# Kernel tuning notes

Measured on AMD Instinct MI355X. Metric: run time of the kernel, lower is better.

Reference implementation:

```python
import jax, jax.numpy as jnp
import numpy as np

PI = float(np.pi)


def setup_inputs() -> dict:
    key = jax.random.key(0)
    ks = jax.random.split(key, 10)
    Nt, Nv, Nx, Nx_out, rank = 1024, 128, 512, 2048, 128
    K = 2 * rank + 1  # 257
    x_sample = jnp.linspace(0.0, 10.0 * PI, Nx, dtype=jnp.float32)
    v_sample = jnp.linspace(-8.0, 8.0, Nv, dtype=jnp.float32)
    x_out = jax.random.uniform(ks[0], (Nx_out,), jnp.float32, 0.0, 10.0 * PI)
    f = jax.random.normal(ks[1], (Nt, Nv, Nx), jnp.float32)
    # psi MLP params (Linear stores W as (out,in) in torch; we use (in,out))
    W1 = jax.random.normal(ks[2], (2, 64), jnp.float32) * 0.5
    b1 = jax.random.normal(ks[3], (64,), jnp.float32) * 0.1
    W2 = jax.random.normal(ks[4], (64, 32), jnp.float32) * 0.125
    b2 = jax.random.normal(ks[5], (32,), jnp.float32) * 0.1
    W3 = jax.random.normal(ks[6], (32, K), jnp.float32) * 0.18
    b3 = jax.random.normal(ks[7], (K,), jnp.float32) * 0.1
    return {"x_out": x_out, "f": f, "x_sample": x_sample, "v_sample": v_sample,
            "W1": W1, "b1": b1, "W2": W2, "b2": b2, "W3": W3, "b3": b3}


def _psi_mlp(xv, W1, b1, W2, b2, W3, b3):
    h = jax.nn.relu(xv @ W1 + b1)
    h = jax.nn.relu(h @ W2 + b2)
    return h @ W3 + b3


def reference(x_out, f, x_sample, v_sample, W1, b1, W2, b2, W3, b3):
    Nt, Nv, Nx = f.shape
    K = W3.shape[1]           # 2*rank + 1
    rank = (K - 1) // 2
    w = 2.0 * PI / (x_sample.max() - x_sample.min())
    hx = x_sample[1] - x_sample[0]
    hv = v_sample[1] - v_sample[0]
    # meshgrid indexing='xy': X, V have shape (Nv, Nx)
    X = jnp.broadcast_to(x_sample[None, :], (Nv, Nx))
    V = jnp.broadcast_to(v_sample[:, None], (Nv, Nx))
    xv = jnp.stack([X.reshape(-1), V.reshape(-1)], axis=1)  # (Nv*Nx, 2)
    Psi = _psi_mlp(xv, W1, b1, W2, b2, W3, b3).reshape(Nv, Nx, K)
    # fused contraction replacing broadcast-multiply-reduce: (Nt,Nv,Nx)x(Nv,Nx,K)->(Nt,K)
    weights = jnp.einsum('tvx,vxk->tk', f, Psi) * (hx * hv)
    ks = jnp.arange(1, rank + 1, dtype=x_out.dtype)
    kc = jnp.arange(0, rank + 1, dtype=x_out.dtype)
    phi = jnp.concatenate([jnp.sin(ks[:, None] * w * x_out[None, :]),
                           jnp.cos(kc[:, None] * w * x_out[None, :])], axis=0)  # (K, Nx_out)
    return weights @ phi  # (Nt, Nx_out)
```

## Files before the change

### kernel.cpp

```cpp
#include <hip/hip_runtime.h>
#include <hip/hip_bf16.h>

typedef short v8s __attribute__((ext_vector_type(8)));
typedef float v4f __attribute__((ext_vector_type(4)));

#define NT   1024
#define NVX  65536
#define KTRUE 257
#define KP   272
#define NXO  2048
#define NJ   48
#define NKC  64

static __device__ __forceinline__ unsigned short f2bf(float f) {
  unsigned int u = __float_as_uint(f);
  u += 0x7FFFu + ((u >> 16) & 1u);
  return (unsigned short)(u >> 16);
}

__global__ void k0_prep(const float* __restrict__ W3, const float* __restrict__ b3,
                        float* __restrict__ W3e) {
  int k = threadIdx.x;
  if (k >= KP) return;
  int j = blockIdx.x;
  float val = 0.f;
  if (k < KTRUE) {
    if (j < 32)       val = W3[j*KTRUE + k];
    else if (j == 32) val = b3[k];
  }
  W3e[j*KP + k] = val;
}

__global__ __launch_bounds__(256) void k1_mlp(
    const float* __restrict__ xs, const float* __restrict__ vs,
    const float* __restrict__ W1, const float* __restrict__ b1,
    const float* __restrict__ W2, const float* __restrict__ b2,
    unsigned short* __restrict__ H2T) {
  int vx = blockIdx.x * 256 + threadIdx.x;
  float x = xs[vx & 511];
  float v = vs[vx >> 9];
  float h2[32];
#pragma unroll
  for (int q = 0; q < 8; ++q) {
    float4 t = ((const float4*)b2)[q];
    h2[q*4+0] = t.x; h2[q*4+1] = t.y; h2[q*4+2] = t.z; h2[q*4+3] = t.w;
  }
#pragma unroll 4
  for (int i = 0; i < 64; ++i) {
    float h1 = fmaf(x, W1[i], fmaf(v, W1[64+i], b1[i]));
    h1 = fmaxf(h1, 0.f);
    const float4* w2r = (const float4*)(W2 + i*32);
#pragma unroll
    for (int q = 0; q < 8; ++q) {
      float4 t = w2r[q];
      h2[q*4+0] = fmaf(h1, t.x, h2[q*4+0]);
      h2[q*4+1] = fmaf(h1, t.y, h2[q*4+1]);
      h2[q*4+2] = fmaf(h1, t.z, h2[q*4+2]);
      h2[q*4+3] = fmaf(h1, t.w, h2[q*4+3]);
    }
  }
#pragma unroll
  for (int j = 0; j < 32; ++j)
    H2T[(size_t)j*NVX + vx] = f2bf(fmaxf(h2[j], 0.f));
  H2T[(size_t)32*NVX + vx] = 0x3F80;
}

__global__ __launch_bounds__(256) void k2_gemm(
    const float* __restrict__ f, const unsigned short* __restrict__ H2T,
    float* __restrict__ Gpart) {
  const int tid  = threadIdx.x;
  const int kc   = blockIdx.x >> 4;
  const int mt   = blockIdx.x & 15;
  const int wave = tid >> 6;
  const int lane = tid & 63;
  const int frow = lane & 15;
  const int kg   = (lane >> 4) * 8;
  const int row  = mt*64 + wave*16 + frow;
  const size_t kbase = (size_t)kc * 1024;

  const float* fp = f + (size_t)row * NVX + kbase + kg;
  const unsigned short* bp0 = H2T + (size_t)(frow)      * NVX + kbase + kg;
  const unsigned short* bp1 = H2T + (size_t)(16 + frow) * NVX + kbase + kg;
  const unsigned short* bp2 = H2T + (size_t)(32 + frow) * NVX + kbase + kg;

  v4f acc0 = {0.f,0.f,0.f,0.f}, acc1 = {0.f,0.f,0.f,0.f}, acc2 = {0.f,0.f,0.f,0.f};

#pragma unroll 4
  for (int step = 0; step < 32; ++step) {
    const int o = step * 32;
    float4 fa = *(const float4*)(fp + o);
    float4 fb = *(const float4*)(fp + o + 4);
    union { v8s v; __hip_bfloat162 h[4]; } au;
    au.h[0] = __float22bfloat162_rn(float2{fa.x, fa.y});
    au.h[1] = __float22bfloat162_rn(float2{fa.z, fa.w});
    au.h[2] = __float22bfloat162_rn(float2{fb.x, fb.y});
    au.h[3] = __float22bfloat162_rn(float2{fb.z, fb.w});
    v8s b0 = *(const v8s*)(bp0 + o);
    v8s b1 = *(const v8s*)(bp1 + o);
    v8s b2 = *(const v8s*)(bp2 + o);
    acc0 = __builtin_amdgcn_mfma_f32_16x16x32_bf16(au.v, b0, acc0, 0, 0, 0);
    acc1 = __builtin_amdgcn_mfma_f32_16x16x32_bf16(au.v, b1, acc1, 0, 0, 0);
    acc2 = __builtin_amdgcn_mfma_f32_16x16x32_bf16(au.v, b2, acc2, 0, 0, 0);
  }

  float* g = Gpart + (size_t)kc * (NT*NJ) + (size_t)(mt*64 + wave*16) * NJ;
  const int r4 = (lane >> 4) * 4;
#pragma unroll
  for (int r = 0; r < 4; ++r) {
    g[(r4 + r)*NJ +      frow] = acc0[r];
    g[(r4 + r)*NJ + 16 + frow] = acc1[r];
    g[(r4 + r)*NJ + 32 + frow] = acc2[r];
  }
}

__global__ __launch_bounds__(256) void k2b_wsum(
    const float* __restrict__ Gpart, const float* __restrict__ W3e,
    const float* __restrict__ xs, const float* __restrict__ vs,
    float* __restrict__ Wsum) {
  __shared__ float gs[4][48];
  const int tid = threadIdx.x, wave = tid >> 6, lane = tid & 63;
  const int t = blockIdx.x * 4 + wave;
  const float scale = (xs[1] - xs[0]) * (vs[1] - vs[0]);
  if (lane < 48) {
    float s = 0.f;
    const float* gp = Gpart + (size_t)t * NJ + lane;
#pragma unroll 8
    for (int kc = 0; kc < NKC; ++kc) s += gp[(size_t)kc * (NT*NJ)];
    gs[wave][lane] = s;
  }
  __syncthreads();
#pragma unroll
  for (int i = 0; i < 5; ++i) {
    int k = lane + i*64;
    if (k < KP) {
      float acc = 0.f;
#pragma unroll
      for (int j = 0; j < 33; ++j) acc = fmaf(gs[wave][j], W3e[j*KP + k], acc);
      Wsum[(size_t)t*KP + k] = acc * scale;
    }
  }
}

__global__ __launch_bounds__(256) void k2c_phi(const float* __restrict__ x_out,
                                               const float* __restrict__ xs,
                                               float* __restrict__ phi) {
  int idx = blockIdx.x * 256 + threadIdx.x;
  int k = idx >> 11, xo = idx & 2047;
  float wmul = 6.283185307179586f / (xs[511] - xs[0]);
  float x = x_out[xo];
  float val;
  if (k < 128)        val = sinf((float)(k+1) * wmul * x);
  else if (k < KTRUE) val = cosf((float)(k-128) * wmul * x);
  else                val = 0.f;
  phi[idx] = val;
}

__global__ __launch_bounds__(256) void k3_out(
    const float* __restrict__ Wsum, const float* __restrict__ phi,
    float* __restrict__ out) {
  __shared__ float At[16][32];
  __shared__ float Bp[16*132];
  const int tid = threadIdx.x;
  const int bt = blockIdx.x >> 4;
  const int bx = blockIdx.x & 15;
  const int t0 = bt*32, xo0 = bx*128;
  const int tr = tid >> 4, tc = tid & 15;
  float acc[2][8];
#pragma unroll
  for (int r = 0; r < 2; ++r)
#pragma unroll
    for (int c = 0; c < 8; ++c) acc[r][c] = 0.f;

  for (int ks = 0; ks < 17; ++ks) {
    int k0 = ks * 16;
    {
      int r = tid & 31, kq = tid >> 5;
      float2 tA = *(const float2*)(Wsum + (size_t)(t0 + r)*KP + k0 + kq*2);
      At[kq*2+0][r] = tA.x;
      At[kq*2+1][r] = tA.y;
    }
#pragma unroll
    for (int it = 0; it < 2; ++it) {
      int q = tid + it*256;
      int kk = q >> 5, c4 = (q & 31) * 4;
      float4 tB = *(const float4*)(phi + (size_t)(k0 + kk)*NXO + xo0 + c4);
      int tcb = c4 >> 3, sub = c4 & 7;
      *(float4*)&Bp[tcb*132 + kk*8 + sub] = tB;
    }
    __syncthreads();
#pragma unroll
    for (int kk = 0; kk < 16; ++kk) {
      float a0 = At[kk][tr*2], a1 = At[kk][tr*2+1];
      float4 b0 = *(const float4*)&Bp[tc*132 + kk*8];
      float4 b1 = *(const float4*)&Bp[tc*132 + kk*8 + 4];
      float b[8] = {b0.x, b0.y, b0.z, b0.w, b1.x, b1.y, b1.z, b1.w};
#pragma unroll
      for (int c = 0; c < 8; ++c) {
        acc[0][c] = fmaf(a0, b[c], acc[0][c]);
        acc[1][c] = fmaf(a1, b[c], acc[1][c]);
      }
    }
    __syncthreads();
  }
#pragma unroll
  for (int r = 0; r < 2; ++r) {
    float4 o0 = {acc[r][0], acc[r][1], acc[r][2], acc[r][3]};
    float4 o1 = {acc[r][4], acc[r][5], acc[r][6], acc[r][7]};
    float* orow = out + (size_t)(t0 + tr*2 + r)*NXO + xo0 + tc*8;
    *(float4*)(orow)     = o0;
    *(float4*)(orow + 4) = o1;
  }
}

extern "C" void kernel_launch(void* const* d_in, const int* in_sizes, int n_in,
                              void* d_out, int out_size, void* d_ws, size_t ws_size,
                              hipStream_t stream) {
  (void)in_sizes; (void)n_in; (void)out_size; (void)ws_size;
  const float* x_out = (const float*)d_in[0];
  const float* f     = (const float*)d_in[1];
  const float* xs    = (const float*)d_in[2];
  const float* vs    = (const float*)d_in[3];
  const float* W1    = (const float*)d_in[4];
  const float* b1    = (const float*)d_in[5];
  const float* W2    = (const float*)d_in[6];
  const float* b2    = (const float*)d_in[7];
  const float* W3    = (const float*)d_in[8];
  const float* b3    = (const float*)d_in[9];
  float* out = (float*)d_out;
  char* ws = (char*)d_ws;

  unsigned short* H2T = (unsigned short*)(ws);
  float* Gpart = (float*)(ws + 6291456);
  float* Wsum  = (float*)(ws + 18874368);
  float* W3e   = (float*)(ws + 19988480);
  float* phi   = (float*)(ws + 20040704);

  hipLaunchKernelGGL(k0_prep,  dim3(48),   dim3(320), 0, stream, W3, b3, W3e);
  hipLaunchKernelGGL(k1_mlp,   dim3(256),  dim3(256), 0, stream, xs, vs, W1, b1, W2, b2, H2T);
  hipLaunchKernelGGL(k2c_phi,  dim3(2176), dim3(256), 0, stream, x_out, xs, phi);
  hipLaunchKernelGGL(k2_gemm,  dim3(1024), dim3(256), 0, stream, f, H2T, Gpart);
  hipLaunchKernelGGL(k2b_wsum, dim3(256),  dim3(256), 0, stream, Gpart, W3e, xs, vs, Wsum);
  hipLaunchKernelGGL(k3_out,   dim3(512),  dim3(256), 0, stream, Wsum, phi, out);
}
```

Measured before the change: 467.6 us.

## Pack MLP features for coalesced MFMA loads, atomically reduce partials, drop bias column

The hidden-feature matrix is now written in a fragment-packed layout, so each lane in the GEMM reads one contiguous 16-byte chunk. The bias column is no longer stored as an all-ones row. Instead, the GEMM computes row sums of f in fp32 and uses two MFMAs per step instead of three. Per-chunk partial results are accumulated into a small buffer with atomicAdd, replacing the large Gpart buffer and its 64-way reduction pass. Other changes: W3 and b3 are read directly, so the prep kernel is removed, and phi is built with one sincos per frequency. Atomics add contention and make the summation order nondeterministic, and __sincosf trades accuracy for speed.

```diff
diff --git a/kernel.cpp b/kernel.cpp
--- a/kernel.cpp
+++ b/kernel.cpp
@@ -4,13 +4,13 @@
 typedef short v8s __attribute__((ext_vector_type(8)));
 typedef float v4f __attribute__((ext_vector_type(4)));
 
-#define NT   1024
-#define NVX  65536
+#define NT    1024
+#define NVX   65536
 #define KTRUE 257
-#define KP   272
-#define NXO  2048
-#define NJ   48
-#define NKC  64
+#define KP    272
+#define NXO   2048
+#define NJG   33
+#define NKC   64
 
 static __device__ __forceinline__ unsigned short f2bf(float f) {
   unsigned int u = __float_as_uint(f);
@@ -18,25 +18,13 @@
   return (unsigned short)(u >> 16);
 }
 
-__global__ void k0_prep(const float* __restrict__ W3, const float* __restrict__ b3,
-                        float* __restrict__ W3e) {
-  int k = threadIdx.x;
-  if (k >= KP) return;
-  int j = blockIdx.x;
-  float val = 0.f;
-  if (k < KTRUE) {
-    if (j < 32)       val = W3[j*KTRUE + k];
-    else if (j == 32) val = b3[k];
-  }
-  W3e[j*KP + k] = val;
-}
-
 __global__ __launch_bounds__(256) void k1_mlp(
     const float* __restrict__ xs, const float* __restrict__ vs,
     const float* __restrict__ W1, const float* __restrict__ b1,
     const float* __restrict__ W2, const float* __restrict__ b2,
-    unsigned short* __restrict__ H2T) {
+    unsigned short* __restrict__ Bpk, float* __restrict__ Gsum) {
   int vx = blockIdx.x * 256 + threadIdx.x;
+  if (vx < NT * NJG) Gsum[vx] = 0.f;
   float x = xs[vx & 511];
   float v = vs[vx >> 9];
   float h2[32];
@@ -59,15 +47,16 @@
       h2[q*4+3] = fmaf(h1, t.w, h2[q*4+3]);
     }
   }
+  size_t base = ((size_t)(vx >> 10) * 32 + ((vx >> 5) & 31)) * 1024
+              + (size_t)((vx >> 3) & 3) * 128 + (vx & 7);
 #pragma unroll
   for (int j = 0; j < 32; ++j)
-    H2T[(size_t)j*NVX + vx] = f2bf(fmaxf(h2[j], 0.f));
-  H2T[(size_t)32*NVX + vx] = 0x3F80;
+    Bpk[base + (size_t)(j >> 4) * 512 + (size_t)(j & 15) * 8] = f2bf(fmaxf(h2[j], 0.f));
 }
 
 __global__ __launch_bounds__(256) void k2_gemm(
-    const float* __restrict__ f, const unsigned short* __restrict__ H2T,
-    float* __restrict__ Gpart) {
+    const float* __restrict__ f, const unsigned short* __restrict__ Bpk,
+    float* __restrict__ Gsum) {
   const int tid  = threadIdx.x;
   const int kc   = blockIdx.x >> 4;
   const int mt   = blockIdx.x & 15;
@@ -75,19 +64,20 @@
   const int lane = tid & 63;
   const int frow = lane & 15;
   const int kg   = (lane >> 4) * 8;
-  const int row  = mt*64 + wave*16 + frow;
+  const int wrow0 = mt*64 + wave*16;
+  const int row  = wrow0 + frow;
   const size_t kbase = (size_t)kc * 1024;
 
   const float* fp = f + (size_t)row * NVX + kbase + kg;
-  const unsigned short* bp0 = H2T + (size_t)(frow)      * NVX + kbase + kg;
-  const unsigned short* bp1 = H2T + (size_t)(16 + frow) * NVX + kbase + kg;
-  const unsigned short* bp2 = H2T + (size_t)(32 + frow) * NVX + kbase + kg;
-
-  v4f acc0 = {0.f,0.f,0.f,0.f}, acc1 = {0.f,0.f,0.f,0.f}, acc2 = {0.f,0.f,0.f,0.f};
+  const unsigned short* bq = Bpk + (size_t)kc * 32768 + (size_t)lane * 8;
+
+  v4f acc0 = {0.f,0.f,0.f,0.f}, acc1 = {0.f,0.f,0.f,0.f};
+  float rs = 0.f;
 
 #pragma unroll 4
   for (int step = 0; step < 32; ++step) {
-    const int o = step * 32;
+    const int o  = step * 32;
+    const int ob = step * 1024;
     float4 fa = *(const float4*)(fp + o);
     float4 fb = *(const float4*)(fp + o + 4);
     union { v8s v; __hip_bfloat162 h[4]; } au;
@@ -95,48 +85,47 @@
     au.h[1] = __float22bfloat162_rn(float2{fa.z, fa.w});
     au.h[2] = __float22bfloat162_rn(float2{fb.x, fb.y});
     au.h[3] = __float22bfloat162_rn(float2{fb.z, fb.w});
-    v8s b0 = *(const v8s*)(bp0 + o);
-    v8s b1 = *(const v8s*)(bp1 + o);
-    v8s b2 = *(const v8s*)(bp2 + o);
+    rs += fa.x + fa.y + fa.z + fa.w + fb.x + fb.y + fb.z + fb.w;
+    v8s b0 = *(const v8s*)(bq + ob);
+    v8s b1 = *(const v8s*)(bq + ob + 512);
     acc0 = __builtin_amdgcn_mfma_f32_16x16x32_bf16(au.v, b0, acc0, 0, 0, 0);
     acc1 = __builtin_amdgcn_mfma_f32_16x16x32_bf16(au.v, b1, acc1, 0, 0, 0);
-    acc2 = __builtin_amdgcn_mfma_f32_16x16x32_bf16(au.v, b2, acc2, 0, 0, 0);
-  }
-
-  float* g = Gpart + (size_t)kc * (NT*NJ) + (size_t)(mt*64 + wave*16) * NJ;
+  }
+
+  rs += __shfl_xor(rs, 16);
+  rs += __shfl_xor(rs, 32);
+
   const int r4 = (lane >> 4) * 4;
 #pragma unroll
   for (int r = 0; r < 4; ++r) {
-    g[(r4 + r)*NJ +      frow] = acc0[r];
-    g[(r4 + r)*NJ + 16 + frow] = acc1[r];
-    g[(r4 + r)*NJ + 32 + frow] = acc2[r];
-  }
+    atomicAdd(&Gsum[(size_t)(wrow0 + r4 + r)*NJG + frow],      acc0[r]);
+    atomicAdd(&Gsum[(size_t)(wrow0 + r4 + r)*NJG + 16 + frow], acc1[r]);
+  }
+  if (lane < 16) atomicAdd(&Gsum[(size_t)row*NJG + 32], rs);
 }
 
 __global__ __launch_bounds__(256) void k2b_wsum(
-    const float* __restrict__ Gpart, const float* __restrict__ W3e,
-    const float* __restrict__ xs, const float* __restrict__ vs,
-    float* __restrict__ Wsum) {
-  __shared__ float gs[4][48];
+    const float* __restrict__ Gsum, const float* __restrict__ W3,
+    const float* __restrict__ b3, const float* __restrict__ xs,
+    const float* __restrict__ vs, float* __restrict__ Wsum) {
+  __shared__ float gs[4][NJG];
   const int tid = threadIdx.x, wave = tid >> 6, lane = tid & 63;
   const int t = blockIdx.x * 4 + wave;
   const float scale = (xs[1] - xs[0]) * (vs[1] - vs[0]);
-  if (lane < 48) {
-    float s = 0.f;
-    const float* gp = Gpart + (size_t)t * NJ + lane;
-#pragma unroll 8
-    for (int kc = 0; kc < NKC; ++kc) s += gp[(size_t)kc * (NT*NJ)];
-    gs[wave][lane] = s;
-  }
+  if (lane < NJG) gs[wave][lane] = Gsum[(size_t)t*NJG + lane];
   __syncthreads();
 #pragma unroll
   for (int i = 0; i < 5; ++i) {
     int k = lane + i*64;
     if (k < KP) {
-      float acc = 0.f;
-#pragma unroll
-      for (int j = 0; j < 33; ++j) acc = fmaf(gs[wave][j], W3e[j*KP + k], acc);
-      Wsum[(size_t)t*KP + k] = acc * scale;
+      float val = 0.f;
+      if (k < KTRUE) {
+        float acc = gs[wave][32] * b3[k];
+#pragma unroll
+        for (int j = 0; j < 32; ++j) acc = fmaf(gs[wave][j], W3[j*KTRUE + k], acc);
+        val = acc * scale;
+      }
+      Wsum[(size_t)t*KP + k] = val;
     }
   }
 }
@@ -145,14 +134,14 @@
                                                const float* __restrict__ xs,
                                                float* __restrict__ phi) {
   int idx = blockIdx.x * 256 + threadIdx.x;
-  int k = idx >> 11, xo = idx & 2047;
+  int fq = idx >> 11, xo = idx & 2047;
   float wmul = 6.283185307179586f / (xs[511] - xs[0]);
   float x = x_out[xo];
-  float val;
-  if (k < 128)        val = sinf((float)(k+1) * wmul * x);
-  else if (k < KTRUE) val = cosf((float)(k-128) * wmul * x);
-  else                val = 0.f;
-  phi[idx] = val;
+  float s, c;
+  __sincosf((float)fq * wmul * x, &s, &c);
+  phi[(size_t)(128 + fq)*NXO + xo] = c;
+  if (fq >= 1) phi[(size_t)(fq - 1)*NXO + xo] = s;
+  if (idx < 15*NXO) phi[(size_t)KTRUE*NXO + idx] = 0.f;
 }
 
 __global__ __launch_bounds__(256) void k3_out(
@@ -229,16 +218,14 @@
   float* out = (float*)d_out;
   char* ws = (char*)d_ws;
 
-  unsigned short* H2T = (unsigned short*)(ws);
-  float* Gpart = (float*)(ws + 6291456);
-  float* Wsum  = (float*)(ws + 18874368);
-  float* W3e   = (float*)(ws + 19988480);
-  float* phi   = (float*)(ws + 20040704);
-
-  hipLaunchKernelGGL(k0_prep,  dim3(48),   dim3(320), 0, stream, W3, b3, W3e);
-  hipLaunchKernelGGL(k1_mlp,   dim3(256),  dim3(256), 0, stream, xs, vs, W1, b1, W2, b2, H2T);
-  hipLaunchKernelGGL(k2c_phi,  dim3(2176), dim3(256), 0, stream, x_out, xs, phi);
-  hipLaunchKernelGGL(k2_gemm,  dim3(1024), dim3(256), 0, stream, f, H2T, Gpart);
-  hipLaunchKernelGGL(k2b_wsum, dim3(256),  dim3(256), 0, stream, Gpart, W3e, xs, vs, Wsum);
+  unsigned short* Bpk = (unsigned short*)(ws);
+  float* Gsum  = (float*)(ws + 4194304);
+  float* Wsum  = (float*)(ws + 4329472);
+  float* phi   = (float*)(ws + 5443584);
+
+  hipLaunchKernelGGL(k1_mlp,   dim3(256),  dim3(256), 0, stream, xs, vs, W1, b1, W2, b2, Bpk, Gsum);
+  hipLaunchKernelGGL(k2c_phi,  dim3(1032), dim3(256), 0, stream, x_out, xs, phi);
+  hipLaunchKernelGGL(k2_gemm,  dim3(1024), dim3(256), 0, stream, f, Bpk, Gsum);
+  hipLaunchKernelGGL(k2b_wsum, dim3(256),  dim3(256), 0, stream, Gsum, W3, b3, xs, vs, Wsum);
   hipLaunchKernelGGL(k3_out,   dim3(512),  dim3(256), 0, stream, Wsum, phi, out);
 }
```

Result: faster. 455.7 us (-2.5%).
